# Kernel optimization log

Hardware: AMD Instinct MI355X
Metric: run time of the kernel (lower is better)

Reference implementation:

```python
import jax, jax.numpy as jnp
import numpy as np

B, N, D, OUT = 8, 2048, 128, 128


def setup_inputs() -> dict:
    key = jax.random.key(0)
    k1, k2, kk, kv, ko, kb = jax.random.split(key, 6)
    x1 = jax.random.normal(k1, (B, N, D), dtype=jnp.float32)
    x2 = jax.random.normal(k2, (B, N, D), dtype=jnp.float32)
    # torch Linear weight layout: [out_features, in_features]; xavier_normal std
    std_k = np.sqrt(2.0 / (D + D))
    Wk = jax.random.normal(kk, (D, D), dtype=jnp.float32) * std_k
    Wv = jax.random.normal(kv, (D, D), dtype=jnp.float32) * std_k
    std_o = np.sqrt(1.0 / D)
    Wo = jax.random.uniform(ko, (OUT, D), dtype=jnp.float32, minval=-std_o, maxval=std_o)
    bo = jax.random.uniform(kb, (OUT,), dtype=jnp.float32, minval=-std_o, maxval=std_o)
    return {"x1": x1, "x2": x2, "Wk": Wk, "Wv": Wv, "Wo": Wo, "bo": bo}


def reference(x1, x2, Wk, Wv, Wo, bo):
    # key projections (no bias)
    h1 = jnp.einsum('bnd,kd->bnk', x1, Wk)  # [B,N1,D]
    h2 = jnp.einsum('bmd,kd->bmk', x2, Wk)  # [B,N2,D]
    e12 = jnp.einsum('bnk,bmk->bnm', h1, h2)  # [B,N1,N2]
    e21 = jnp.einsum('bmk,bnk->bmn', h2, h1)  # [B,N2,N1]
    # NOTE: original uses Softmax(dim=1), i.e. over the QUERY axis — faithful here.
    a12 = jax.nn.softmax(e12, axis=1)
    a21 = jax.nn.softmax(e21, axis=1)
    v2 = jnp.einsum('bmd,kd->bmk', x2, Wv)
    v1 = jnp.einsum('bnd,kd->bnk', x1, Wv)
    n12 = jnp.einsum('bnm,bmk->bnk', a12, v2)  # [B,N1,D]
    n21 = jnp.einsum('bmn,bnk->bmk', a21, v1)  # [B,N2,D]
    msg1 = jax.nn.leaky_relu(jnp.einsum('bnk,ok->bno', n12, Wo) + bo, 0.01)
    msg2 = jax.nn.leaky_relu(jnp.einsum('bmk,ok->bmo', n21, Wo) + bo, 0.01)
    return (msg1, msg2)
```

## Files before the change

kernel.cpp:

```cpp
#include <hip/hip_runtime.h>
#include <hip/hip_bf16.h>

#define B_ 8
#define N_ 2048
#define D_ 128
#define CFIX 95.0f

typedef __attribute__((ext_vector_type(8))) _Float16 half8;
typedef __attribute__((ext_vector_type(8))) unsigned short ushort8;
typedef __attribute__((ext_vector_type(4))) float floatx4;
typedef __attribute__((ext_vector_type(16))) float floatx16;

__device__ __forceinline__ unsigned short f2h(float f) {
    _Float16 h = (_Float16)f;
    union { _Float16 h; unsigned short u; } v; v.h = h;
    return v.u;
}
__device__ __forceinline__ ushort4 f2h4(float4 f) {
    ushort4 u; u.x = f2h(f.x); u.y = f2h(f.y); u.z = f2h(f.z); u.w = f2h(f.w);
    return u;
}
__device__ __forceinline__ half8 mk_half8(unsigned int a, unsigned int b,
                                          unsigned int c, unsigned int d) {
    union { unsigned int u[4]; half8 h; } v;
    v.u[0] = a; v.u[1] = b; v.u[2] = c; v.u[3] = d;
    return v.h;
}
__device__ __forceinline__ void plswap(unsigned int &x, unsigned int &y, int hi) {
    unsigned int sx = (unsigned int)__shfl_xor((int)x, 32, 64);
    unsigned int sy = (unsigned int)__shfl_xor((int)y, 32, 64);
    x = hi ? sy : x;
    y = hi ? y : sx;
}

__global__ __launch_bounds__(256)
void proj_kernel(const float* __restrict__ x1, const float* __restrict__ x2,
                 const float* __restrict__ Wk, const float* __restrict__ Wv,
                 unsigned short* __restrict__ h1, unsigned short* __restrict__ h2,
                 unsigned short* __restrict__ v1t, unsigned short* __restrict__ v2t,
                 float* __restrict__ sums)
{
    __shared__ unsigned short Xs[64][136];
    __shared__ unsigned short Ws[128][136];
    const int which = blockIdx.y;
    const float* x = (which & 1) ? x2 : x1;
    const float* W = (which & 2) ? Wv : Wk;
    const int rowbase = blockIdx.x * 64;
    const int t = threadIdx.x;

    {
        int base = (blockIdx.y * 256 + blockIdx.x) * 32;
        if (t < 32) sums[base + t] = 0.0f;
    }

    for (int it = 0; it < 8; ++it) {
        int idx = t + 256 * it;
        int r = idx >> 5, c = (idx & 31) * 4;
        float4 f = *(const float4*)(x + (size_t)(rowbase + r) * 128 + c);
        *(ushort4*)&Xs[r][c] = f2h4(f);
    }
    for (int it = 0; it < 16; ++it) {
        int idx = t + 256 * it;
        int r = idx >> 5, c = (idx & 31) * 4;
        float4 f = *(const float4*)(W + (size_t)r * 128 + c);
        *(ushort4*)&Ws[r][c] = f2h4(f);
    }
    __syncthreads();

    const int lane = t & 63, wave = t >> 6, l15 = lane & 15, quad = lane >> 4;
    half8 a[4];
    for (int ks = 0; ks < 4; ++ks)
        a[ks] = *(const half8*)&Xs[wave * 16 + l15][ks * 32 + quad * 8];
    __syncthreads();

    if (which < 2) {
        unsigned short* out = which ? h2 : h1;
        for (int c = 0; c < 8; ++c) {
            floatx4 acc = {0.f, 0.f, 0.f, 0.f};
            for (int ks = 0; ks < 4; ++ks) {
                half8 b = *(const half8*)&Ws[c * 16 + l15][ks * 32 + quad * 8];
                acc = __builtin_amdgcn_mfma_f32_16x16x32_f16(a[ks], b, acc, 0, 0, 0);
            }
            int col = c * 16 + l15;
            for (int r = 0; r < 4; ++r)
                Xs[wave * 16 + quad * 4 + r][col] = f2h(acc[r]);
        }
        __syncthreads();
        for (int i = 0; i < 4; ++i) {
            int idx = t + 256 * i;
            int r = idx >> 4, c8 = idx & 15;
            ushort8 v = *(const ushort8*)&Xs[r][c8 * 8];
            *(ushort8*)(out + (size_t)(rowbase + r) * 128 + c8 * 8) = v;
        }
    } else {
        unsigned short* vt = (which == 2) ? v1t : v2t;
        unsigned short (*Xt)[68] = (unsigned short (*)[68])&Xs[0][0];
        for (int c = 0; c < 8; ++c) {
            floatx4 acc = {0.f, 0.f, 0.f, 0.f};
            for (int ks = 0; ks < 4; ++ks) {
                half8 b = *(const half8*)&Ws[c * 16 + l15][ks * 32 + quad * 8];
                acc = __builtin_amdgcn_mfma_f32_16x16x32_f16(a[ks], b, acc, 0, 0, 0);
            }
            int col = c * 16 + l15;
            for (int r = 0; r < 4; ++r)
                Xt[col][wave * 16 + quad * 4 + r] = f2h(acc[r]);
        }
        __syncthreads();
        const int bb = rowbase >> 11;
        const int n0 = rowbase & (N_ - 1);
        for (int i = 0; i < 8; ++i) {
            int idx = t + 256 * i;
            int d = idx >> 4, q4 = idx & 15;
            ushort4 v = *(const ushort4*)&Xt[d][q4 * 4];
            *(ushort4*)(vt + ((size_t)bb * 128 + d) * N_ + n0 + q4 * 4) = v;
        }
    }
}

__global__ __launch_bounds__(512, 4)
void stats_kernel(const unsigned short* __restrict__ h1g, const unsigned short* __restrict__ h2g,
                  float* __restrict__ rsum, float* __restrict__ csum)
{
    __shared__ unsigned short Ks[2][64][136];
    __shared__ float colpart[4][1024];
    const int b = blockIdx.y, qbase = blockIdx.x * 64, keybase = blockIdx.z * 1024;
    const int t = threadIdx.x;
    const unsigned short* Q = h1g + (size_t)b * N_ * 128;
    const unsigned short* K = h2g + (size_t)b * N_ * 128;

    for (int i = 0; i < 8; ++i)
        colpart[0][t + 512 * i] = 0.f;

    const int lane = t & 63, wave = t >> 6, l15 = lane & 15, quad = lane >> 4;
    const int g = wave >> 1, s = wave & 1;

    half8 a[4];
    for (int ks = 0; ks < 4; ++ks)
        a[ks] = *(const half8*)(Q + (size_t)(qbase + g * 16 + l15) * 128 + ks * 32 + quad * 8);

    int krow[2], kc8[2];
    half8 kreg[2];
    for (int it = 0; it < 2; ++it) {
        int idx = t + 512 * it;
        krow[it] = idx >> 4; kc8[it] = idx & 15;
    }
    for (int it = 0; it < 2; ++it)
        kreg[it] = *(const half8*)(K + (size_t)(keybase + krow[it]) * 128 + kc8[it] * 8);
    for (int it = 0; it < 2; ++it)
        *(half8*)&Ks[0][krow[it]][kc8[it] * 8] = kreg[it];
    for (int it = 0; it < 2; ++it)
        kreg[it] = *(const half8*)(K + (size_t)(keybase + 64 + krow[it]) * 128 + kc8[it] * 8);
    __syncthreads();

    float racc[4] = {0.f, 0.f, 0.f, 0.f};

    for (int kt = 0; kt < 16; ++kt) {
        const int cb = kt & 1;
        for (int it = 0; it < 2; ++it)
            *(half8*)&Ks[cb ^ 1][krow[it]][kc8[it] * 8] = kreg[it];
        int ktp = (kt + 2 < 16) ? kt + 2 : 15;
        for (int it = 0; it < 2; ++it)
            kreg[it] = *(const half8*)(K + (size_t)(keybase + ktp * 64 + krow[it]) * 128 + kc8[it] * 8);

        for (int cc = 0; cc < 2; ++cc) {
            int c = 2 * s + cc;
            floatx4 acc = {0.f, 0.f, 0.f, 0.f};
            for (int ks = 0; ks < 4; ++ks) {
                half8 bb = *(const half8*)&Ks[cb][c * 16 + l15][ks * 32 + quad * 8];
                acc = __builtin_amdgcn_mfma_f32_16x16x32_f16(a[ks], bb, acc, 0, 0, 0);
            }
            float e0 = __expf(acc[0] - CFIX), e1 = __expf(acc[1] - CFIX);
            float e2 = __expf(acc[2] - CFIX), e3 = __expf(acc[3] - CFIX);
            racc[0] += e0; racc[1] += e1; racc[2] += e2; racc[3] += e3;
            float cs = e0 + e1 + e2 + e3;
            cs += __shfl_xor(cs, 16, 64);
            cs += __shfl_xor(cs, 32, 64);
            if (quad == 0) colpart[g][kt * 64 + c * 16 + l15] = cs;
        }
        __syncthreads();
    }
    {
        float v0 = colpart[0][t] + colpart[1][t] + colpart[2][t] + colpart[3][t];
        float v1 = colpart[0][t + 512] + colpart[1][t + 512]
                 + colpart[2][t + 512] + colpart[3][t + 512];
        atomicAdd(&csum[(size_t)b * N_ + keybase + t], v0);
        atomicAdd(&csum[(size_t)b * N_ + keybase + t + 512], v1);
    }

    for (int r = 0; r < 4; ++r) {
        float v = racc[r];
        v += __shfl_xor(v, 1, 64);
        v += __shfl_xor(v, 2, 64);
        v += __shfl_xor(v, 4, 64);
        v += __shfl_xor(v, 8, 64);
        if (l15 == 0)
            atomicAdd(&rsum[(size_t)b * N_ + qbase + g * 16 + quad * 4 + r], v);
    }
}

__global__ __launch_bounds__(512)
void log_kernel(float* __restrict__ sums, const float* __restrict__ Wo,
                unsigned short* __restrict__ wo16)
{
    int i = blockIdx.x * 1024 + threadIdx.x * 2;
    float2 v = *(float2*)(sums + i);
    v.x = -(CFIX + __logf(v.x));
    v.y = -(CFIX + __logf(v.y));
    *(float2*)(sums + i) = v;
    if (blockIdx.x < 16) {
        float2 w = *(const float2*)(Wo + i);
        unsigned int pk = (unsigned int)f2h(w.x) | ((unsigned int)f2h(w.y) << 16);
        *(unsigned int*)(wo16 + i) = pk;
    }
}

__global__ __launch_bounds__(512, 2)
void attn_kernel(const unsigned short* __restrict__ h1g, const unsigned short* __restrict__ h2g,
                 const unsigned short* __restrict__ v1tg, const unsigned short* __restrict__ v2tg,
                 const float* __restrict__ rsumL, const float* __restrict__ csumL,
                 const unsigned short* __restrict__ wo16, const float* __restrict__ bo,
                 float* __restrict__ outp, int zbase)
{
    __shared__ __align__(16) unsigned short Ks[2][2][64][136];
    __shared__ __align__(16) unsigned short Vs[2][2][128][72];

    const int bid = blockIdx.x;
    const int b = bid & 7;
    const int qblk = (bid >> 3) & 15;
    const int dir = (bid >> 7) + zbase;
    const int qbase = qblk * 128;

    const unsigned short* Q  = (dir ? h2g : h1g) + (size_t)b * N_ * 128;
    const unsigned short* K  = (dir ? h1g : h2g) + (size_t)b * N_ * 128;
    const unsigned short* VT = (dir ? v1tg : v2tg) + (size_t)b * 128 * N_;
    const float* SL = (dir ? rsumL : csumL) + (size_t)b * N_;
    float* outbase = outp + (dir ? (size_t)B_ * N_ * 128 : 0);

    const int t = threadIdx.x;
    const int lane = t & 63, wave = t >> 6;
    const int l31 = lane & 31, h = lane >> 5;
    const int qt = wave & 3, j = wave >> 2;

    half8 qf[8];
    #pragma unroll
    for (int ds = 0; ds < 8; ++ds)
        qf[ds] = *(const half8*)(Q + (size_t)(qbase + qt * 32 + l31) * 128 + ds * 16 + h * 8);

    int krow[2], kc8[2], vd[2], vc8[2];
    #pragma unroll
    for (int s2 = 0; s2 < 2; ++s2) {
        int idx = t + 512 * s2;
        krow[s2] = idx >> 4; kc8[s2] = idx & 15;
        vd[s2]   = idx >> 3; vc8[s2] = idx & 7;
    }
    half8 kreg[2][2], vreg[2][2];
    #pragma unroll
    for (int jj = 0; jj < 2; ++jj)
        #pragma unroll
        for (int s2 = 0; s2 < 2; ++s2) {
            kreg[jj][s2] = *(const half8*)(K + (size_t)(jj * 1024 + krow[s2]) * 128 + kc8[s2] * 8);
            vreg[jj][s2] = *(const half8*)(VT + (size_t)vd[s2] * N_ + jj * 1024 + vc8[s2] * 8);
        }
    #pragma unroll
    for (int jj = 0; jj < 2; ++jj)
        #pragma unroll
        for (int s2 = 0; s2 < 2; ++s2) {
            *(half8*)&Ks[0][jj][krow[s2]][kc8[s2] * 8] = kreg[jj][s2];
            *(half8*)&Vs[0][jj][vd[s2]][vc8[s2] * 8]   = vreg[jj][s2];
        }
    #pragma unroll
    for (int jj = 0; jj < 2; ++jj)
        #pragma unroll
        for (int s2 = 0; s2 < 2; ++s2) {
            kreg[jj][s2] = *(const half8*)(K + (size_t)(jj * 1024 + 64 + krow[s2]) * 128 + kc8[s2] * 8);
            vreg[jj][s2] = *(const half8*)(VT + (size_t)vd[s2] * N_ + jj * 1024 + 64 + vc8[s2] * 8);
        }
    __syncthreads();

    floatx16 o0 = {}, o1 = {}, o2 = {}, o3 = {};

    for (int kt = 0; kt < 16; ++kt) {
        const int cb = kt & 1;
        #pragma unroll
        for (int jj = 0; jj < 2; ++jj)
            #pragma unroll
            for (int s2 = 0; s2 < 2; ++s2) {
                *(half8*)&Ks[cb ^ 1][jj][krow[s2]][kc8[s2] * 8] = kreg[jj][s2];
                *(half8*)&Vs[cb ^ 1][jj][vd[s2]][vc8[s2] * 8]   = vreg[jj][s2];
            }
        int ktp = (kt + 2 < 16) ? kt + 2 : 15;
        #pragma unroll
        for (int jj = 0; jj < 2; ++jj)
            #pragma unroll
            for (int s2 = 0; s2 < 2; ++s2) {
                kreg[jj][s2] = *(const half8*)(K + (size_t)(jj * 1024 + ktp * 64 + krow[s2]) * 128 + kc8[s2] * 8);
                vreg[jj][s2] = *(const half8*)(VT + (size_t)vd[s2] * N_ + jj * 1024 + ktp * 64 + vc8[s2] * 8);
            }
        #pragma unroll
        for (int ks = 0; ks < 2; ++ks) {
            const int kb = j * 1024 + kt * 64 + ks * 32;
            float4 L0 = *(const float4*)(SL + kb + 4 * h);
            float4 L1 = *(const float4*)(SL + kb + 4 * h + 8);
            float4 L2 = *(const float4*)(SL + kb + 4 * h + 16);
            float4 L3 = *(const float4*)(SL + kb + 4 * h + 24);
            floatx16 acc;
            acc[0] = L0.x; acc[1] = L0.y; acc[2]  = L0.z; acc[3]  = L0.w;
            acc[4] = L1.x; acc[5] = L1.y; acc[6]  = L1.z; acc[7]  = L1.w;
            acc[8] = L2.x; acc[9] = L2.y; acc[10] = L2.z; acc[11] = L2.w;
            acc[12] = L3.x; acc[13] = L3.y; acc[14] = L3.z; acc[15] = L3.w;
            #pragma unroll
            for (int ds = 0; ds < 8; ++ds) {
                half8 kf = *(const half8*)&Ks[cb][j][ks * 32 + l31][ds * 16 + h * 8];
                acc = __builtin_amdgcn_mfma_f32_32x32x16_f16(kf, qf[ds], acc, 0, 0, 0);
            }
            unsigned int c[8];
            #pragma unroll
            for (int p = 0; p < 8; ++p) {
                unsigned int lo  = f2h(__expf(acc[2 * p]));
                unsigned int hi2 = f2h(__expf(acc[2 * p + 1]));
                c[p] = lo | (hi2 << 16);
            }
            plswap(c[0], c[2], h);
            plswap(c[1], c[3], h);
            plswap(c[4], c[6], h);
            plswap(c[5], c[7], h);
            half8 pa0 = mk_half8(c[0], c[1], c[2], c[3]);
            half8 pa1 = mk_half8(c[4], c[5], c[6], c[7]);
            {
                half8 vb;
                vb = *(const half8*)&Vs[cb][j][0 * 32 + l31][ks * 32 + h * 8];
                o0 = __builtin_amdgcn_mfma_f32_32x32x16_f16(pa0, vb, o0, 0, 0, 0);
                vb = *(const half8*)&Vs[cb][j][0 * 32 + l31][ks * 32 + 16 + h * 8];
                o0 = __builtin_amdgcn_mfma_f32_32x32x16_f16(pa1, vb, o0, 0, 0, 0);
                vb = *(const half8*)&Vs[cb][j][1 * 32 + l31][ks * 32 + h * 8];
                o1 = __builtin_amdgcn_mfma_f32_32x32x16_f16(pa0, vb, o1, 0, 0, 0);
                vb = *(const half8*)&Vs[cb][j][1 * 32 + l31][ks * 32 + 16 + h * 8];
                o1 = __builtin_amdgcn_mfma_f32_32x32x16_f16(pa1, vb, o1, 0, 0, 0);
                vb = *(const half8*)&Vs[cb][j][2 * 32 + l31][ks * 32 + h * 8];
                o2 = __builtin_amdgcn_mfma_f32_32x32x16_f16(pa0, vb, o2, 0, 0, 0);
                vb = *(const half8*)&Vs[cb][j][2 * 32 + l31][ks * 32 + 16 + h * 8];
                o2 = __builtin_amdgcn_mfma_f32_32x32x16_f16(pa1, vb, o2, 0, 0, 0);
                vb = *(const half8*)&Vs[cb][j][3 * 32 + l31][ks * 32 + h * 8];
                o3 = __builtin_amdgcn_mfma_f32_32x32x16_f16(pa0, vb, o3, 0, 0, 0);
                vb = *(const half8*)&Vs[cb][j][3 * 32 + l31][ks * 32 + 16 + h * 8];
                o3 = __builtin_amdgcn_mfma_f32_32x32x16_f16(pa1, vb, o3, 0, 0, 0);
            }
        }
        __syncthreads();
    }

    float (*Rbuf)[32][128] = (float (*)[32][128])&Ks[0][0][0][0];
    unsigned short (*Nsq)[32][136] = (unsigned short (*)[32][136])&Vs[0][0][0][0];
    if (j == 1) {
        #pragma unroll
        for (int r = 0; r < 16; ++r) {
            int row = (r & 3) + 8 * (r >> 2) + 4 * h;
            Rbuf[qt][row][0 * 32 + l31] = o0[r];
            Rbuf[qt][row][1 * 32 + l31] = o1[r];
            Rbuf[qt][row][2 * 32 + l31] = o2[r];
            Rbuf[qt][row][3 * 32 + l31] = o3[r];
        }
    }
    __syncthreads();
    if (j == 0) {
        #pragma unroll
        for (int r = 0; r < 16; ++r) {
            int row = (r & 3) + 8 * (r >> 2) + 4 * h;
            Nsq[qt][row][0 * 32 + l31] = f2h(o0[r] + Rbuf[qt][row][0 * 32 + l31]);
            Nsq[qt][row][1 * 32 + l31] = f2h(o1[r] + Rbuf[qt][row][1 * 32 + l31]);
            Nsq[qt][row][2 * 32 + l31] = f2h(o2[r] + Rbuf[qt][row][2 * 32 + l31]);
            Nsq[qt][row][3 * 32 + l31] = f2h(o3[r] + Rbuf[qt][row][3 * 32 + l31]);
        }
    }
    __syncthreads();
    #pragma unroll
    for (int oc = 0; oc < 2; ++oc) {
        const int ob = j * 64 + oc * 32;
        floatx16 acc2 = {};
        #pragma unroll
        for (int ds = 0; ds < 8; ++ds) {
            half8 na = *(const half8*)&Nsq[qt][l31][ds * 16 + h * 8];
            half8 wb = *(const half8*)(wo16 + (size_t)(ob + l31) * 128 + ds * 16 + h * 8);
            acc2 = __builtin_amdgcn_mfma_f32_32x32x16_f16(na, wb, acc2, 0, 0, 0);
        }
        float bias = bo[ob + l31];
        #pragma unroll
        for (int r = 0; r < 16; ++r) {
            int row = (r & 3) + 8 * (r >> 2) + 4 * h;
            float mv = acc2[r] + bias;
            mv = (mv >= 0.0f) ? mv : 0.01f * mv;
            outbase[(size_t)(b * N_ + qbase + qt * 32 + row) * 128 + ob + l31] = mv;
        }
    }
}

extern "C" void kernel_launch(void* const* d_in, const int* in_sizes, int n_in,
                              void* d_out, int out_size, void* d_ws, size_t ws_size,
                              hipStream_t stream)
{
    const float* x1 = (const float*)d_in[0];
    const float* x2 = (const float*)d_in[1];
    const float* Wk = (const float*)d_in[2];
    const float* Wv = (const float*)d_in[3];
    const float* Wo = (const float*)d_in[4];
    const float* bo = (const float*)d_in[5];
    float* out = (float*)d_out;

    const size_t nrow = (size_t)B_ * N_;
    unsigned short* h1  = (unsigned short*)d_ws;
    unsigned short* h2  = h1 + nrow * 128;
    unsigned short* v1t = h2 + nrow * 128;
    const size_t need = 4 * nrow * 128 * sizeof(unsigned short)
                      + 2 * nrow * sizeof(float) + (size_t)128 * 128 * 2;
    const bool fits = ws_size >= need;

    unsigned short* v2t;
    float* rsum;
    if (fits) {
        v2t = v1t + nrow * 128;
        rsum = (float*)(v2t + nrow * 128);
    } else {
        v2t = (unsigned short*)(out + nrow * 128);
        rsum = (float*)(v1t + nrow * 128);
    }
    float* csum = rsum + nrow;
    unsigned short* wo16 = (unsigned short*)(csum + nrow);

    proj_kernel<<<dim3(256, 4), 256, 0, stream>>>(x1, x2, Wk, Wv, h1, h2, v1t, v2t, rsum);
    stats_kernel<<<dim3(32, 8, 2), 512, 0, stream>>>(h1, h2, rsum, csum);
    log_kernel<<<dim3(32), 512, 0, stream>>>(rsum, Wo, wo16);
    if (fits) {
        attn_kernel<<<dim3(256), 512, 0, stream>>>(h1, h2, v1t, v2t, rsum, csum,
                                                   wo16, bo, out, 0);
    } else {
        attn_kernel<<<dim3(128), 512, 0, stream>>>(h1, h2, v1t, v2t, rsum, csum,
                                                   wo16, bo, out, 0);
        attn_kernel<<<dim3(128), 512, 0, stream>>>(h1, h2, v1t, v2t, rsum, csum,
                                                   wo16, bo, out, 1);
    }
}
```

Before: 153.5 us.

## Compute row and column softmax sums via separate transposed passes with 32x32 MFMA

The stats kernel no longer accumulates column sums through shared-memory partials and cross-wave reductions. It now runs two directions (h1 vs h2 and h2 vs h1), each producing row sums only, and uses 32x32x16 MFMA with the -CFIX offset folded into the accumulator's initial value. This removes the colpart LDS traffic and shuffles but doubles the QK^T matmul work, and it changes occupancy and the grid shape.

```diff
diff --git a/kernel.cpp b/kernel.cpp
--- a/kernel.cpp
+++ b/kernel.cpp
@@ -117,85 +117,97 @@
     }
 }
 
-__global__ __launch_bounds__(512, 4)
+__global__ __launch_bounds__(512, 2)
 void stats_kernel(const unsigned short* __restrict__ h1g, const unsigned short* __restrict__ h2g,
                   float* __restrict__ rsum, float* __restrict__ csum)
 {
-    __shared__ unsigned short Ks[2][64][136];
-    __shared__ float colpart[4][1024];
-    const int b = blockIdx.y, qbase = blockIdx.x * 64, keybase = blockIdx.z * 1024;
+    __shared__ __align__(16) unsigned short Ks[2][2][64][136];
+
+    const int bid = blockIdx.x;
+    const int b = bid & 7;
+    const int qblk = (bid >> 3) & 15;
+    const int dir = bid >> 7;
+    const int qbase = qblk * 128;
+
+    const unsigned short* Q = (dir ? h2g : h1g) + (size_t)b * N_ * 128;
+    const unsigned short* K = (dir ? h1g : h2g) + (size_t)b * N_ * 128;
+    float* outp = (dir ? csum : rsum) + (size_t)b * N_;
+
     const int t = threadIdx.x;
-    const unsigned short* Q = h1g + (size_t)b * N_ * 128;
-    const unsigned short* K = h2g + (size_t)b * N_ * 128;
-
-    for (int i = 0; i < 8; ++i)
-        colpart[0][t + 512 * i] = 0.f;
-
-    const int lane = t & 63, wave = t >> 6, l15 = lane & 15, quad = lane >> 4;
-    const int g = wave >> 1, s = wave & 1;
-
-    half8 a[4];
-    for (int ks = 0; ks < 4; ++ks)
-        a[ks] = *(const half8*)(Q + (size_t)(qbase + g * 16 + l15) * 128 + ks * 32 + quad * 8);
+    const int lane = t & 63, wave = t >> 6;
+    const int l31 = lane & 31, h = lane >> 5;
+    const int qt = wave & 3, j = wave >> 2;
+
+    half8 qf[8];
+    #pragma unroll
+    for (int ds = 0; ds < 8; ++ds)
+        qf[ds] = *(const half8*)(Q + (size_t)(qbase + qt * 32 + l31) * 128 + ds * 16 + h * 8);
 
     int krow[2], kc8[2];
-    half8 kreg[2];
-    for (int it = 0; it < 2; ++it) {
-        int idx = t + 512 * it;
-        krow[it] = idx >> 4; kc8[it] = idx & 15;
-    }
-    for (int it = 0; it < 2; ++it)
-        kreg[it] = *(const half8*)(K + (size_t)(keybase + krow[it]) * 128 + kc8[it] * 8);
-    for (int it = 0; it < 2; ++it)
-        *(half8*)&Ks[0][krow[it]][kc8[it] * 8] = kreg[it];
-    for (int it = 0; it < 2; ++it)
-        kreg[it] = *(const half8*)(K + (size_t)(keybase + 64 + krow[it]) * 128 + kc8[it] * 8);
-    __syncthreads();
-
-    float racc[4] = {0.f, 0.f, 0.f, 0.f};
+    #pragma unroll
+    for (int s2 = 0; s2 < 2; ++s2) {
+        int idx = t + 512 * s2;
+        krow[s2] = idx >> 4; kc8[s2] = idx & 15;
+    }
+    half8 kreg[2][2];
+    #pragma unroll
+    for (int jj = 0; jj < 2; ++jj)
+        #pragma unroll
+        for (int s2 = 0; s2 < 2; ++s2)
+            kreg[jj][s2] = *(const half8*)(K + (size_t)(jj * 1024 + krow[s2]) * 128 + kc8[s2] * 8);
+    #pragma unroll
+    for (int jj = 0; jj < 2; ++jj)
+        #pragma unroll
+        for (int s2 = 0; s2 < 2; ++s2)
+            *(half8*)&Ks[0][jj][krow[s2]][kc8[s2] * 8] = kreg[jj][s2];
+    #pragma unroll
+    for (int jj = 0; jj < 2; ++jj)
+        #pragma unroll
+        for (int s2 = 0; s2 < 2; ++s2)
+            kreg[jj][s2] = *(const half8*)(K + (size_t)(jj * 1024 + 64 + krow[s2]) * 128 + kc8[s2] * 8);
+    __syncthreads();
+
+    float racc = 0.0f;
 
     for (int kt = 0; kt < 16; ++kt) {
         const int cb = kt & 1;
-        for (int it = 0; it < 2; ++it)
-            *(half8*)&Ks[cb ^ 1][krow[it]][kc8[it] * 8] = kreg[it];
+        #pragma unroll
+        for (int jj = 0; jj < 2; ++jj)
+            #pragma unroll
+            for (int s2 = 0; s2 < 2; ++s2)
+                *(half8*)&Ks[cb ^ 1][jj][krow[s2]][kc8[s2] * 8] = kreg[jj][s2];
         int ktp = (kt + 2 < 16) ? kt + 2 : 15;
-        for (int it = 0; it < 2; ++it)
-            kreg[it] = *(const half8*)(K + (size_t)(keybase + ktp * 64 + krow[it]) * 128 + kc8[it] * 8);
-
-        for (int cc = 0; cc < 2; ++cc) {
-            int c = 2 * s + cc;
-            floatx4 acc = {0.f, 0.f, 0.f, 0.f};
-            for (int ks = 0; ks < 4; ++ks) {
-                half8 bb = *(const half8*)&Ks[cb][c * 16 + l15][ks * 32 + quad * 8];
-                acc = __builtin_amdgcn_mfma_f32_16x16x32_f16(a[ks], bb, acc, 0, 0, 0);
-            }
-            float e0 = __expf(acc[0] - CFIX), e1 = __expf(acc[1] - CFIX);
-            float e2 = __expf(acc[2] - CFIX), e3 = __expf(acc[3] - CFIX);
-            racc[0] += e0; racc[1] += e1; racc[2] += e2; racc[3] += e3;
-            float cs = e0 + e1 + e2 + e3;
-            cs += __shfl_xor(cs, 16, 64);
-            cs += __shfl_xor(cs, 32, 64);
-            if (quad == 0) colpart[g][kt * 64 + c * 16 + l15] = cs;
+        #pragma unroll
+        for (int jj = 0; jj < 2; ++jj)
+            #pragma unroll
+            for (int s2 = 0; s2 < 2; ++s2)
+                kreg[jj][s2] = *(const half8*)(K + (size_t)(jj * 1024 + ktp * 64 + krow[s2]) * 128 + kc8[s2] * 8);
+
+        #pragma unroll
+        for (int ks = 0; ks < 2; ++ks) {
+            floatx16 acc;
+            #pragma unroll
+            for (int r = 0; r < 16; ++r) acc[r] = -CFIX;
+            #pragma unroll
+            for (int ds = 0; ds < 8; ++ds) {
+                half8 kf = *(const half8*)&Ks[cb][j][ks * 32 + l31][ds * 16 + h * 8];
+                acc = __builtin_amdgcn_mfma_f32_32x32x16_f16(kf, qf[ds], acc, 0, 0, 0);
+            }
+            float e[16];
+            #pragma unroll
+            for (int r = 0; r < 16; ++r) e[r] = __expf(acc[r]);
+            #pragma unroll
+            for (int st = 8; st > 0; st >>= 1)
+                #pragma unroll
+                for (int r = 0; r < st; ++r) e[r] += e[r + st];
+            racc += e[0];
         }
         __syncthreads();
     }
-    {
-        float v0 = colpart[0][t] + colpart[1][t] + colpart[2][t] + colpart[3][t];
-        float v1 = colpart[0][t + 512] + colpart[1][t + 512]
-                 + colpart[2][t + 512] + colpart[3][t + 512];
-        atomicAdd(&csum[(size_t)b * N_ + keybase + t], v0);
-        atomicAdd(&csum[(size_t)b * N_ + keybase + t + 512], v1);
-    }
-
-    for (int r = 0; r < 4; ++r) {
-        float v = racc[r];
-        v += __shfl_xor(v, 1, 64);
-        v += __shfl_xor(v, 2, 64);
-        v += __shfl_xor(v, 4, 64);
-        v += __shfl_xor(v, 8, 64);
-        if (l15 == 0)
-            atomicAdd(&rsum[(size_t)b * N_ + qbase + g * 16 + quad * 4 + r], v);
-    }
+
+    racc += __shfl_xor(racc, 32, 64);
+    if (h == 0)
+        atomicAdd(&outp[qbase + qt * 32 + l31], racc);
 }
 
 __global__ __launch_bounds__(512)
@@ -427,7 +439,7 @@
     unsigned short* wo16 = (unsigned short*)(csum + nrow);
 
     proj_kernel<<<dim3(256, 4), 256, 0, stream>>>(x1, x2, Wk, Wv, h1, h2, v1t, v2t, rsum);
-    stats_kernel<<<dim3(32, 8, 2), 512, 0, stream>>>(h1, h2, rsum, csum);
+    stats_kernel<<<dim3(256), 512, 0, stream>>>(h1, h2, rsum, csum);
     log_kernel<<<dim3(32), 512, 0, stream>>>(rsum, Wo, wo16);
     if (fits) {
         attn_kernel<<<dim3(256), 512, 0, stream>>>(h1, h2, v1t, v2t, rsum, csum,
```

Result: no change. 153.7 us (+0.1%).
